# Performance work log

Measured on AMD Instinct MI355X. Metric: run time of the kernel, lower is better.

## Reference

```python
import jax, jax.numpy as jnp
import numpy as np

DIM = 192
HEADS = 6
WS = (4, 8, 8)  # window size (D, H, W)
N = WS[0] * WS[1] * WS[2]  # 256 tokens per window
NW = 64
B_ = 256  # batch * nW


def _relative_position_index(ws):
    d, h, w = ws
    coords = jnp.stack(jnp.meshgrid(jnp.arange(d), jnp.arange(h), jnp.arange(w), indexing='ij'))
    coords = coords.reshape(3, -1)  # (3, N)
    rel = coords[:, :, None] - coords[:, None, :]  # (3, N, N)
    rel = rel.transpose(1, 2, 0) + jnp.array([d - 1, h - 1, w - 1])
    idx = rel[..., 0] * ((2 * h - 1) * (2 * w - 1)) + rel[..., 1] * (2 * w - 1) + rel[..., 2]
    return idx.astype(jnp.int32)  # (N, N)


def setup_inputs() -> dict:
    key = jax.random.key(0)
    ks = jax.random.split(key, 7)
    table_rows = (2 * WS[0] - 1) * (2 * WS[1] - 1) * (2 * WS[2] - 1)  # 1575
    return {
        'x': jax.random.normal(ks[0], (B_, N, DIM), dtype=jnp.float32),
        'mask': jax.random.normal(ks[1], (NW, N, N), dtype=jnp.float32),
        'qkv_w': jax.random.normal(ks[2], (DIM, 3 * DIM), dtype=jnp.float32) * 0.02,
        'qkv_b': jnp.zeros((3 * DIM,), dtype=jnp.float32),
        'proj_w': jax.random.normal(ks[3], (DIM, DIM), dtype=jnp.float32) * 0.02,
        'proj_b': jnp.zeros((DIM,), dtype=jnp.float32),
        'bias_table': jax.random.normal(ks[4], (table_rows, HEADS), dtype=jnp.float32) * 0.02,
        'rel_index': _relative_position_index(WS),
    }


def reference(x, mask, qkv_w, qkv_b, proj_w, proj_b, bias_table, rel_index):
    B, Ntok, C = x.shape
    hd = C // HEADS
    scale = hd ** (-0.5)
    qkv = (x @ qkv_w + qkv_b).reshape(B, Ntok, 3, HEADS, hd)
    qkv = qkv.transpose(2, 0, 3, 1, 4)  # (3, B, H, N, hd)
    q, k, v = qkv[0], qkv[1], qkv[2]
    attn = jnp.einsum('bhnd,bhmd->bhnm', q * scale, k)  # (B, H, N, N)
    # gathered relative-position bias: (N, N, H) -> (H, N, N)
    bias = bias_table[rel_index.reshape(-1)].reshape(Ntok, Ntok, HEADS).transpose(2, 0, 1)
    attn = attn + bias[None]
    nW = mask.shape[0]
    attn = attn.reshape(B // nW, nW, HEADS, Ntok, Ntok) + mask[None, :, None]
    attn = attn.reshape(B, HEADS, Ntok, Ntok)
    attn = jax.nn.softmax(attn, axis=-1)
    out = jnp.einsum('bhnm,bhmd->bhnd', attn, v)  # (B, H, N, hd)
    out = out.transpose(0, 2, 1, 3).reshape(B, Ntok, C)
    out = out @ proj_w + proj_b
    return out
```

## Files before the change

kernel.cpp:

```cpp
#include <hip/hip_runtime.h>
#include <cstdint>
#include <math.h>

#define DIMC 192
#define NTOK 256
#define HEADS 6
#define HD 32

typedef __bf16 bf16x8 __attribute__((ext_vector_type(8)));
typedef __bf16 bf16x4 __attribute__((ext_vector_type(4)));
typedef float f32x4 __attribute__((ext_vector_type(4)));

__device__ __forceinline__ void gload_lds16(const __bf16* g, __bf16* l) {
    __builtin_amdgcn_global_load_lds((const __attribute__((address_space(1))) void*)g,
                                     (__attribute__((address_space(3))) void*)l, 16, 0, 0);
}

__global__ void cast_x(const float* __restrict__ x, __bf16* __restrict__ xb) {
    int i = blockIdx.x * 256 + threadIdx.x;
    float4 a = ((const float4*)x)[i * 2];
    float4 b = ((const float4*)x)[i * 2 + 1];
    bf16x8 o = {(__bf16)a.x, (__bf16)a.y, (__bf16)a.z, (__bf16)a.w,
                (__bf16)b.x, (__bf16)b.y, (__bf16)b.z, (__bf16)b.w};
    ((bf16x8*)xb)[i] = o;
}

__global__ void transcast(const float* __restrict__ w, __bf16* __restrict__ wt, int K, int N) {
    int i = blockIdx.x * 256 + threadIdx.x;
    int n = i / K, k = i - n * K;
    wt[i] = (__bf16)w[(size_t)k * N + n];
}

__global__ void biasb_kernel(const float* __restrict__ table, const int* __restrict__ rel,
                             __bf16* __restrict__ biasb) {
    int i = blockIdx.x * 256 + threadIdx.x;
    int h = i >> 16;
    int r = i & 65535;
    biasb[i] = (__bf16)table[rel[r] * 6 + h];
}

__global__ void bm_kernel(const float* __restrict__ mask, const __bf16* __restrict__ biasb,
                          __bf16* __restrict__ bm) {
    int i = blockIdx.x * 256 + threadIdx.x;
    int w = i >> 13, oct = i & 8191;
    float4 m0 = ((const float4*)mask)[(size_t)w * 16384 + oct * 2];
    float4 m1 = ((const float4*)mask)[(size_t)w * 16384 + oct * 2 + 1];
    #pragma unroll
    for (int h = 0; h < 6; ++h) {
        bf16x8 bb = ((const bf16x8*)biasb)[h * 8192 + oct];
        bf16x8 o = {(__bf16)(m0.x + (float)bb[0]), (__bf16)(m0.y + (float)bb[1]),
                    (__bf16)(m0.z + (float)bb[2]), (__bf16)(m0.w + (float)bb[3]),
                    (__bf16)(m1.x + (float)bb[4]), (__bf16)(m1.y + (float)bb[5]),
                    (__bf16)(m1.z + (float)bb[6]), (__bf16)(m1.w + (float)bb[7])};
        ((bf16x8*)bm)[(size_t)(w * 6 + h) * 8192 + oct] = o;
    }
}

__launch_bounds__(256, 2)
__global__ void qkv_mfma(const __bf16* __restrict__ A, const __bf16* __restrict__ Wt,
                         const float* __restrict__ bias,
                         __bf16* __restrict__ qo, __bf16* __restrict__ ko, __bf16* __restrict__ vo) {
    __shared__ __bf16 As[256 * 64];
    __shared__ __bf16 Bs[96 * 64];
    const int t = threadIdx.x;
    const int wv = t >> 6, lane = t & 63;
    const int l16 = lane & 15, quad = lane >> 4;

    const int lin = blockIdx.x + blockIdx.y * 6;
    const int xcd = lin & 7, pos = lin >> 3;
    const int bx = pos % 6;
    const int by = xcd + (pos / 6) * 8;

    const int m0 = by * 256;
    const int j0 = bx * 96;

    f32x4 acc[4][6];
    #pragma unroll
    for (int mt = 0; mt < 4; ++mt)
        #pragma unroll
        for (int nt = 0; nt < 6; ++nt)
            acc[mt][nt] = (f32x4){0.f, 0.f, 0.f, 0.f};

    for (int kit = 0; kit < 3; ++kit) {
        const int k0 = kit * 64;
        #pragma unroll
        for (int gi = 0; gi < 8; ++gi) {
            int g = wv * 8 + gi;
            int cid = g * 64 + lane;
            int row = cid >> 3, kcs = cid & 7;
            int kcg = kcs ^ (row & 7);
            gload_lds16(A + (size_t)(m0 + row) * DIMC + k0 + kcg * 8, As + g * 512);
        }
        #pragma unroll
        for (int gi = 0; gi < 3; ++gi) {
            int g = wv * 3 + gi;
            int cid = g * 64 + lane;
            int n = cid >> 3, kcs = cid & 7;
            int kcg = kcs ^ (n & 7);
            gload_lds16(Wt + (size_t)(j0 + n) * DIMC + k0 + kcg * 8, Bs + g * 512);
        }
        __syncthreads();
        #pragma unroll
        for (int kk = 0; kk < 2; ++kk) {
            bf16x8 af[4], bfr[6];
            #pragma unroll
            for (int mt = 0; mt < 4; ++mt) {
                int row = wv * 64 + mt * 16 + l16;
                int ch = (kk * 4 + quad) ^ (row & 7);
                af[mt] = *(const bf16x8*)(As + row * 64 + ch * 8);
            }
            #pragma unroll
            for (int nt = 0; nt < 6; ++nt) {
                int n = nt * 16 + l16;
                int ch = (kk * 4 + quad) ^ (n & 7);
                bfr[nt] = *(const bf16x8*)(Bs + n * 64 + ch * 8);
            }
            #pragma unroll
            for (int mt = 0; mt < 4; ++mt)
                #pragma unroll
                for (int nt = 0; nt < 6; ++nt)
                    acc[mt][nt] = __builtin_amdgcn_mfma_f32_16x16x32_bf16(af[mt], bfr[nt], acc[mt][nt], 0, 0, 0);
        }
        __syncthreads();
    }

    const int which = bx >> 1;
    __bf16* outp = which == 0 ? qo : (which == 1 ? ko : vo);
    const float sc = which == 0 ? 0.17677669529663687f : 1.0f;
    float bq[6];
    #pragma unroll
    for (int nt = 0; nt < 6; ++nt) bq[nt] = bias[j0 + nt * 16 + l16];
    const int cloc = (bx & 1) * 96;
    __bf16* tile = As + wv * 4096;
    const int TP = 104;
    #pragma unroll
    for (int mt = 0; mt < 4; ++mt) {
        #pragma unroll
        for (int nt = 0; nt < 6; ++nt)
            #pragma unroll
            for (int r = 0; r < 4; ++r)
                tile[(quad * 4 + r) * TP + nt * 16 + l16] = (__bf16)((acc[mt][nt][r] + bq[nt]) * sc);
        int row = lane >> 2;
        #pragma unroll
        for (int it = 0; it < 3; ++it) {
            int c8 = (lane & 3) + it * 4;
            bf16x8 val = *(const bf16x8*)(tile + row * TP + c8 * 8);
            int token = m0 + wv * 64 + mt * 16 + row;
            int b = token >> 8, n = token & 255;
            int cw = cloc + c8 * 8;
            int h = cw >> 5, d0 = cw & 31;
            *(bf16x8*)(outp + (((size_t)b * HEADS + h) * NTOK + n) * HD + d0) = val;
        }
    }
}

__launch_bounds__(256, 3)
__global__ void attn_mfma(const __bf16* __restrict__ qg, const __bf16* __restrict__ kg,
                          const __bf16* __restrict__ vg, const __bf16* __restrict__ bm,
                          __bf16* __restrict__ aout) {
    __shared__ __bf16 Ks[NTOK][40];
    __shared__ __bf16 VTs[HD][264];
    __shared__ __bf16 Ps[4][16][40];
    __shared__ float  Sums[4][64];

    const int lin = blockIdx.x;
    const int xcd = lin & 7, pos = lin >> 3;
    const int g = xcd + (pos >> 2) * 8;
    const int i4 = pos & 3;
    const int h = g % 6, w = g / 6;
    const int b = i4 * 64 + w;
    const int bh = b * HEADS + h;

    const int t = threadIdx.x;
    const size_t base = (size_t)bh * (NTOK * HD);

    #pragma unroll
    for (int it = 0; it < 4; ++it) {
        int c = t + 256 * it;
        int row = c >> 2, off = c & 3;
        *(uint4*)(&Ks[row][off * 8]) = *(const uint4*)(kg + base + row * HD + off * 8);
    }
    #pragma unroll
    for (int it = 0; it < 4; ++it) {
        int d0 = it * 8;
        bf16x8 vv = *(const bf16x8*)(vg + base + t * HD + d0);
        #pragma unroll
        for (int j = 0; j < 8; ++j)
            VTs[d0 + j][t] = vv[j];
    }
    __syncthreads();

    const int wv = t >> 6, lane = t & 63;
    const int l16 = lane & 15, quad = lane >> 4;
    const int q0 = wv * 64;

    bf16x8 qf[4];
    #pragma unroll
    for (int qt = 0; qt < 4; ++qt)
        qf[qt] = *(const bf16x8*)(qg + base + (size_t)(q0 + qt * 16 + l16) * HD + quad * 8);

    f32x4 o[4][2];
    #pragma unroll
    for (int qt = 0; qt < 4; ++qt)
        #pragma unroll
        for (int dt = 0; dt < 2; ++dt)
            o[qt][dt] = (f32x4){0.f, 0.f, 0.f, 0.f};
    float rsum[4] = {};

    const __bf16* bmq = bm + (size_t)(w * 6 + h) * 65536 + (size_t)(q0 + l16) * 256 + quad * 4;

    for (int c = 0; c < 8; ++c) {
        const int kb = c * 32;
        bf16x4 bmv[4][2];
        #pragma unroll
        for (int qt = 0; qt < 4; ++qt)
            #pragma unroll
            for (int kt = 0; kt < 2; ++kt)
                bmv[qt][kt] = *(const bf16x4*)(bmq + qt * 4096 + kb + kt * 16);
        bf16x8 kf[2];
        #pragma unroll
        for (int kt = 0; kt < 2; ++kt)
            kf[kt] = *(const bf16x8*)(&Ks[kb + kt * 16 + l16][quad * 8]);
        bf16x8 vf[2];
        #pragma unroll
        for (int dt = 0; dt < 2; ++dt)
            vf[dt] = *(const bf16x8*)(&VTs[dt * 16 + l16][kb + quad * 8]);

        #pragma unroll
        for (int qt = 0; qt < 4; ++qt) {
            #pragma unroll
            for (int kt = 0; kt < 2; ++kt) {
                f32x4 s = (f32x4){0.f, 0.f, 0.f, 0.f};
                s = __builtin_amdgcn_mfma_f32_16x16x32_bf16(kf[kt], qf[qt], s, 0, 0, 0);
                bf16x4 pk;
                #pragma unroll
                for (int r = 0; r < 4; ++r) {
                    float p = __expf(s[r] + (float)bmv[qt][kt][r]);
                    rsum[qt] += p;
                    pk[r] = (__bf16)p;
                }
                *(bf16x4*)(&Ps[wv][l16][kt * 16 + quad * 4]) = pk;
            }
            bf16x8 pf = *(const bf16x8*)(&Ps[wv][l16][quad * 8]);
            #pragma unroll
            for (int dt = 0; dt < 2; ++dt)
                o[qt][dt] = __builtin_amdgcn_mfma_f32_16x16x32_bf16(pf, vf[dt], o[qt][dt], 0, 0, 0);
        }
    }

    #pragma unroll
    for (int qt = 0; qt < 4; ++qt) {
        float s = rsum[qt];
        s += __shfl_xor(s, 16);
        s += __shfl_xor(s, 32);
        if (quad == 0) Sums[wv][qt * 16 + l16] = 1.0f / s;
    }
    #pragma unroll
    for (int qt = 0; qt < 4; ++qt) {
        f32x4 inv = *(const f32x4*)(&Sums[wv][qt * 16 + quad * 4]);
        #pragma unroll
        for (int dt = 0; dt < 2; ++dt)
            #pragma unroll
            for (int r = 0; r < 4; ++r) {
                int qrow = q0 + qt * 16 + quad * 4 + r;
                aout[((size_t)b * NTOK + qrow) * DIMC + h * HD + dt * 16 + l16] =
                    (__bf16)(o[qt][dt][r] * inv[r]);
            }
    }
}

__launch_bounds__(256, 2)
__global__ void proj_mfma(const __bf16* __restrict__ A, const __bf16* __restrict__ Wt,
                          const float* __restrict__ bias, float* __restrict__ out) {
    __shared__ __bf16 As[256 * 64];
    __shared__ __bf16 Bs[96 * 64];
    const int t = threadIdx.x;
    const int wv = t >> 6, lane = t & 63;
    const int l16 = lane & 15, quad = lane >> 4;

    const int lin = blockIdx.x + blockIdx.y * 2;
    const int xcd = lin & 7, pos = lin >> 3;
    const int bx = pos & 1;
    const int by = xcd + (pos >> 1) * 8;

    const int m0 = by * 256;
    const int j0 = bx * 96;

    f32x4 acc[4][6];
    #pragma unroll
    for (int mt = 0; mt < 4; ++mt)
        #pragma unroll
        for (int nt = 0; nt < 6; ++nt)
            acc[mt][nt] = (f32x4){0.f, 0.f, 0.f, 0.f};

    for (int kit = 0; kit < 3; ++kit) {
        const int k0 = kit * 64;
        #pragma unroll
        for (int gi = 0; gi < 8; ++gi) {
            int g = wv * 8 + gi;
            int cid = g * 64 + lane;
            int row = cid >> 3, kcs = cid & 7;
            int kcg = kcs ^ (row & 7);
            gload_lds16(A + (size_t)(m0 + row) * DIMC + k0 + kcg * 8, As + g * 512);
        }
        #pragma unroll
        for (int gi = 0; gi < 3; ++gi) {
            int g = wv * 3 + gi;
            int cid = g * 64 + lane;
            int n = cid >> 3, kcs = cid & 7;
            int kcg = kcs ^ (n & 7);
            gload_lds16(Wt + (size_t)(j0 + n) * DIMC + k0 + kcg * 8, Bs + g * 512);
        }
        __syncthreads();
        #pragma unroll
        for (int kk = 0; kk < 2; ++kk) {
            bf16x8 af[4], bfr[6];
            #pragma unroll
            for (int mt = 0; mt < 4; ++mt) {
                int row = wv * 64 + mt * 16 + l16;
                int ch = (kk * 4 + quad) ^ (row & 7);
                af[mt] = *(const bf16x8*)(As + row * 64 + ch * 8);
            }
            #pragma unroll
            for (int nt = 0; nt < 6; ++nt) {
                int n = nt * 16 + l16;
                int ch = (kk * 4 + quad) ^ (n & 7);
                bfr[nt] = *(const bf16x8*)(Bs + n * 64 + ch * 8);
            }
            #pragma unroll
            for (int mt = 0; mt < 4; ++mt)
                #pragma unroll
                for (int nt = 0; nt < 6; ++nt)
                    acc[mt][nt] = __builtin_amdgcn_mfma_f32_16x16x32_bf16(af[mt], bfr[nt], acc[mt][nt], 0, 0, 0);
        }
        __syncthreads();
    }

    #pragma unroll
    for (int nt = 0; nt < 6; ++nt) {
        int colg = j0 + nt * 16 + l16;
        float bv = bias[colg];
        #pragma unroll
        for (int mt = 0; mt < 4; ++mt)
            #pragma unroll
            for (int r = 0; r < 4; ++r) {
                int token = m0 + wv * 64 + mt * 16 + quad * 4 + r;
                out[(size_t)token * DIMC + colg] = acc[mt][nt][r] + bv;
            }
    }
}

extern "C" void kernel_launch(void* const* d_in, const int* in_sizes, int n_in,
                              void* d_out, int out_size, void* d_ws, size_t ws_size,
                              hipStream_t stream) {
    const float* x          = (const float*)d_in[0];
    const float* mask       = (const float*)d_in[1];
    const float* qkv_w      = (const float*)d_in[2];
    const float* qkv_b      = (const float*)d_in[3];
    const float* proj_w     = (const float*)d_in[4];
    const float* proj_b     = (const float*)d_in[5];
    const float* bias_table = (const float*)d_in[6];
    const int*   rel_index  = (const int*)d_in[7];

    char* ws = (char*)d_ws;
    __bf16* xb    = (__bf16*)(ws);
    __bf16* q     = (__bf16*)(ws + 25165824);
    __bf16* k     = (__bf16*)(ws + 50331648);
    __bf16* v     = (__bf16*)(ws + 75497472);
    __bf16* biasb = (__bf16*)(ws + 100663296);
    __bf16* wqt   = (__bf16*)(ws + 102236160);
    __bf16* wpt   = (__bf16*)(ws + 102457344);
    __bf16* aoutb = xb;
    __bf16* bm    = (__bf16*)d_out;

    cast_x<<<6144, 256, 0, stream>>>(x, xb);
    transcast<<<432, 256, 0, stream>>>(qkv_w, wqt, DIMC, 576);
    transcast<<<144, 256, 0, stream>>>(proj_w, wpt, DIMC, DIMC);
    biasb_kernel<<<1536, 256, 0, stream>>>(bias_table, rel_index, biasb);
    bm_kernel<<<2048, 256, 0, stream>>>(mask, biasb, bm);
    qkv_mfma<<<dim3(6, 256), 256, 0, stream>>>(xb, wqt, qkv_b, q, k, v);
    attn_mfma<<<1536, 256, 0, stream>>>(q, k, v, bm, aoutb);
    proj_mfma<<<dim3(2, 256), 256, 0, stream>>>(aoutb, wpt, proj_b, (float*)d_out);
}
```

Measured before the change: 235.9 us.

## Merge prep kernels, fuse mask build into QKV launch, use exp2 softmax

Four small preprocessing kernels are merged into one launch, and the mask+bias build is added as extra blocks of the QKV GEMM launch, cutting the launch count from eight to four. Log2(e) is folded into the query scale, bias and mask so the softmax can use the hardware exp2 instruction directly. The mask tile loads in the attention loop are also software-prefetched one chunk ahead. This adds register pressure in the attention kernel, and the fused QKV launch now mixes heterogeneous blocks that all reserve the GEMM's shared memory.

```diff
diff --git a/kernel.cpp b/kernel.cpp
--- a/kernel.cpp
+++ b/kernel.cpp
@@ -6,6 +6,7 @@
 #define NTOK 256
 #define HEADS 6
 #define HD 32
+#define L2E 1.4426950408889634f
 
 typedef __bf16 bf16x8 __attribute__((ext_vector_type(8)));
 typedef __bf16 bf16x4 __attribute__((ext_vector_type(4)));
@@ -16,61 +17,68 @@
                                      (__attribute__((address_space(3))) void*)l, 16, 0, 0);
 }
 
-__global__ void cast_x(const float* __restrict__ x, __bf16* __restrict__ xb) {
-    int i = blockIdx.x * 256 + threadIdx.x;
-    float4 a = ((const float4*)x)[i * 2];
-    float4 b = ((const float4*)x)[i * 2 + 1];
-    bf16x8 o = {(__bf16)a.x, (__bf16)a.y, (__bf16)a.z, (__bf16)a.w,
-                (__bf16)b.x, (__bf16)b.y, (__bf16)b.z, (__bf16)b.w};
-    ((bf16x8*)xb)[i] = o;
-}
-
-__global__ void transcast(const float* __restrict__ w, __bf16* __restrict__ wt, int K, int N) {
-    int i = blockIdx.x * 256 + threadIdx.x;
-    int n = i / K, k = i - n * K;
-    wt[i] = (__bf16)w[(size_t)k * N + n];
-}
-
-__global__ void biasb_kernel(const float* __restrict__ table, const int* __restrict__ rel,
-                             __bf16* __restrict__ biasb) {
-    int i = blockIdx.x * 256 + threadIdx.x;
-    int h = i >> 16;
-    int r = i & 65535;
-    biasb[i] = (__bf16)table[rel[r] * 6 + h];
-}
-
-__global__ void bm_kernel(const float* __restrict__ mask, const __bf16* __restrict__ biasb,
-                          __bf16* __restrict__ bm) {
-    int i = blockIdx.x * 256 + threadIdx.x;
-    int w = i >> 13, oct = i & 8191;
-    float4 m0 = ((const float4*)mask)[(size_t)w * 16384 + oct * 2];
-    float4 m1 = ((const float4*)mask)[(size_t)w * 16384 + oct * 2 + 1];
-    #pragma unroll
-    for (int h = 0; h < 6; ++h) {
-        bf16x8 bb = ((const bf16x8*)biasb)[h * 8192 + oct];
-        bf16x8 o = {(__bf16)(m0.x + (float)bb[0]), (__bf16)(m0.y + (float)bb[1]),
-                    (__bf16)(m0.z + (float)bb[2]), (__bf16)(m0.w + (float)bb[3]),
-                    (__bf16)(m1.x + (float)bb[4]), (__bf16)(m1.y + (float)bb[5]),
-                    (__bf16)(m1.z + (float)bb[6]), (__bf16)(m1.w + (float)bb[7])};
-        ((bf16x8*)bm)[(size_t)(w * 6 + h) * 8192 + oct] = o;
+__global__ void prep(const float* __restrict__ x, __bf16* __restrict__ xb,
+                     const float* __restrict__ qkv_w, __bf16* __restrict__ wqt,
+                     const float* __restrict__ proj_w, __bf16* __restrict__ wpt,
+                     const float* __restrict__ table, const int* __restrict__ rel,
+                     __bf16* __restrict__ biasb) {
+    const int bid = blockIdx.x, t = threadIdx.x;
+    if (bid < 6144) {
+        int i = bid * 256 + t;
+        float4 a = ((const float4*)x)[i * 2];
+        float4 b = ((const float4*)x)[i * 2 + 1];
+        bf16x8 o = {(__bf16)a.x, (__bf16)a.y, (__bf16)a.z, (__bf16)a.w,
+                    (__bf16)b.x, (__bf16)b.y, (__bf16)b.z, (__bf16)b.w};
+        ((bf16x8*)xb)[i] = o;
+    } else if (bid < 6576) {
+        int i = (bid - 6144) * 256 + t;
+        int n = i / DIMC, k = i - n * DIMC;
+        wqt[i] = (__bf16)qkv_w[(size_t)k * 576 + n];
+    } else if (bid < 6720) {
+        int i = (bid - 6576) * 256 + t;
+        int n = i / DIMC, k = i - n * DIMC;
+        wpt[i] = (__bf16)proj_w[(size_t)k * DIMC + n];
+    } else {
+        int i = (bid - 6720) * 256 + t;
+        int h = i >> 16;
+        int r = i & 65535;
+        biasb[i] = (__bf16)(table[rel[r] * 6 + h] * L2E);
     }
 }
 
 __launch_bounds__(256, 2)
-__global__ void qkv_mfma(const __bf16* __restrict__ A, const __bf16* __restrict__ Wt,
-                         const float* __restrict__ bias,
-                         __bf16* __restrict__ qo, __bf16* __restrict__ ko, __bf16* __restrict__ vo) {
+__global__ void qkvbm(const __bf16* __restrict__ A, const __bf16* __restrict__ Wt,
+                      const float* __restrict__ bias,
+                      __bf16* __restrict__ qo, __bf16* __restrict__ ko, __bf16* __restrict__ vo,
+                      const float* __restrict__ mask, const __bf16* __restrict__ biasb,
+                      __bf16* __restrict__ bm) {
     __shared__ __bf16 As[256 * 64];
     __shared__ __bf16 Bs[96 * 64];
     const int t = threadIdx.x;
+    const int lin = blockIdx.x;
+
+    if (lin >= 1536) {
+        int i = (lin - 1536) * 256 + t;
+        int w = i >> 13, oct = i & 8191;
+        float4 m0 = ((const float4*)mask)[(size_t)w * 16384 + oct * 2];
+        float4 m1 = ((const float4*)mask)[(size_t)w * 16384 + oct * 2 + 1];
+        #pragma unroll
+        for (int h = 0; h < 6; ++h) {
+            bf16x8 bb = ((const bf16x8*)biasb)[h * 8192 + oct];
+            bf16x8 o = {(__bf16)(m0.x * L2E + (float)bb[0]), (__bf16)(m0.y * L2E + (float)bb[1]),
+                        (__bf16)(m0.z * L2E + (float)bb[2]), (__bf16)(m0.w * L2E + (float)bb[3]),
+                        (__bf16)(m1.x * L2E + (float)bb[4]), (__bf16)(m1.y * L2E + (float)bb[5]),
+                        (__bf16)(m1.z * L2E + (float)bb[6]), (__bf16)(m1.w * L2E + (float)bb[7])};
+            ((bf16x8*)bm)[(size_t)(w * 6 + h) * 8192 + oct] = o;
+        }
+        return;
+    }
+
     const int wv = t >> 6, lane = t & 63;
     const int l16 = lane & 15, quad = lane >> 4;
-
-    const int lin = blockIdx.x + blockIdx.y * 6;
     const int xcd = lin & 7, pos = lin >> 3;
     const int bx = pos % 6;
     const int by = xcd + (pos / 6) * 8;
-
     const int m0 = by * 256;
     const int j0 = bx * 96;
 
@@ -126,7 +134,7 @@
 
     const int which = bx >> 1;
     __bf16* outp = which == 0 ? qo : (which == 1 ? ko : vo);
-    const float sc = which == 0 ? 0.17677669529663687f : 1.0f;
+    const float sc = which == 0 ? (0.17677669529663687f * L2E) : 1.0f;
     float bq[6];
     #pragma unroll
     for (int nt = 0; nt < 6; ++nt) bq[nt] = bias[j0 + nt * 16 + l16];
@@ -209,14 +217,23 @@
 
     const __bf16* bmq = bm + (size_t)(w * 6 + h) * 65536 + (size_t)(q0 + l16) * 256 + quad * 4;
 
+    bf16x4 bmv[4][2];
+    #pragma unroll
+    for (int qt = 0; qt < 4; ++qt)
+        #pragma unroll
+        for (int kt = 0; kt < 2; ++kt)
+            bmv[qt][kt] = *(const bf16x4*)(bmq + qt * 4096 + kt * 16);
+
     for (int c = 0; c < 8; ++c) {
         const int kb = c * 32;
-        bf16x4 bmv[4][2];
-        #pragma unroll
-        for (int qt = 0; qt < 4; ++qt)
-            #pragma unroll
-            for (int kt = 0; kt < 2; ++kt)
-                bmv[qt][kt] = *(const bf16x4*)(bmq + qt * 4096 + kb + kt * 16);
+        bf16x4 bmn[4][2];
+        if (c < 7) {
+            #pragma unroll
+            for (int qt = 0; qt < 4; ++qt)
+                #pragma unroll
+                for (int kt = 0; kt < 2; ++kt)
+                    bmn[qt][kt] = *(const bf16x4*)(bmq + qt * 4096 + kb + 32 + kt * 16);
+        }
         bf16x8 kf[2];
         #pragma unroll
         for (int kt = 0; kt < 2; ++kt)
@@ -235,7 +252,7 @@
                 bf16x4 pk;
                 #pragma unroll
                 for (int r = 0; r < 4; ++r) {
-                    float p = __expf(s[r] + (float)bmv[qt][kt][r]);
+                    float p = __builtin_amdgcn_exp2f(s[r] + (float)bmv[qt][kt][r]);
                     rsum[qt] += p;
                     pk[r] = (__bf16)p;
                 }
@@ -245,6 +262,13 @@
             #pragma unroll
             for (int dt = 0; dt < 2; ++dt)
                 o[qt][dt] = __builtin_amdgcn_mfma_f32_16x16x32_bf16(pf, vf[dt], o[qt][dt], 0, 0, 0);
+        }
+        if (c < 7) {
+            #pragma unroll
+            for (int qt = 0; qt < 4; ++qt)
+                #pragma unroll
+                for (int kt = 0; kt < 2; ++kt)
+                    bmv[qt][kt] = bmn[qt][kt];
         }
     }
 
@@ -373,12 +397,8 @@
     __bf16* aoutb = xb;
     __bf16* bm    = (__bf16*)d_out;
 
-    cast_x<<<6144, 256, 0, stream>>>(x, xb);
-    transcast<<<432, 256, 0, stream>>>(qkv_w, wqt, DIMC, 576);
-    transcast<<<144, 256, 0, stream>>>(proj_w, wpt, DIMC, DIMC);
-    biasb_kernel<<<1536, 256, 0, stream>>>(bias_table, rel_index, biasb);
-    bm_kernel<<<2048, 256, 0, stream>>>(mask, biasb, bm);
-    qkv_mfma<<<dim3(6, 256), 256, 0, stream>>>(xb, wqt, qkv_b, q, k, v);
+    prep<<<8256, 256, 0, stream>>>(x, xb, qkv_w, wqt, proj_w, wpt, bias_table, rel_index, biasb);
+    qkvbm<<<3584, 256, 0, stream>>>(xb, wqt, qkv_b, q, k, v, mask, biasb, bm);
     attn_mfma<<<1536, 256, 0, stream>>>(q, k, v, bm, aoutb);
     proj_mfma<<<dim3(2, 256), 256, 0, stream>>>(aoutb, wpt, proj_b, (float*)d_out);
 }
```

Measured after the change: 221.4 us. -6.1%, faster.
